# Performance work log

Measured on AMD Instinct MI355X. Metric: run time of the kernel, lower is better.

Reference implementation:

```python
import jax, jax.numpy as jnp
import numpy as np

B, N, R, VR = 4, 10475, 48, 96


def setup_inputs() -> dict:
    key = jax.random.key(0)
    k1, k2, k3, k4 = jax.random.split(key, 4)
    v1s = jax.random.normal(k1, (B, N, 3), dtype=jnp.float32)
    v2s = jax.random.normal(k2, (B, N, 3), dtype=jnp.float32)
    cmaps = jax.random.randint(k3, (B, R, R), 0, 2).astype(bool)
    rid_to_vid = jax.random.randint(k4, (R, VR), 0, N, dtype=jnp.int32)
    return {"v1s": v1s, "v2s": v2s, "cmaps": cmaps, "rid_to_vid": rid_to_vid}


def reference(v1s, v2s, cmaps, rid_to_vid):
    # Gather region vertex subsets for ALL regions at once: [B, R, Vr, 3]
    g1 = v1s[:, rid_to_vid, :]
    g2 = v2s[:, rid_to_vid, :]
    # Squared norms per point
    sq1 = jnp.sum(g1 * g1, axis=-1)                 # [B, R, Vr]
    sq2 = jnp.sum(g2 * g2, axis=-1)                 # [B, R, Vr]
    # Inner products for every (region r of person1, region s of person2) pair
    inner = jnp.einsum('brvc,bswc->brsvw', g1, g2)  # [B, R, R, Vr, Vr]
    d2 = sq1[:, :, None, :, None] + sq2[:, None, :, None, :] - 2.0 * inner
    d = jnp.sqrt(jnp.maximum(d2, 0.0))              # squared=False -> euclidean
    # min over the two vertex-subset axes -> per region-pair min distance [B, R, R]
    min_d = jnp.min(d, axis=(3, 4))
    # Original averages min dists only over active contact pairs (torch.where(cmap))
    m = cmaps.astype(min_d.dtype)                   # [B, R, R]
    return jnp.sum(min_d * m, axis=(1, 2)) / jnp.sum(m, axis=(1, 2))
```

## Files before the change

### kernel.cpp

```cpp
#include <hip/hip_runtime.h>

#define B_ 4
#define R_ 48
#define VR_ 96
#define NROWS (B_ * 2 * R_)
#define ROWF 288

__global__ __launch_bounds__(256) void gather_kernel(
    const float* __restrict__ v1s, const float* __restrict__ v2s,
    const int* __restrict__ rid_to_vid, float* __restrict__ gbuf, int N) {
  const int i = blockIdx.x * 256 + threadIdx.x;
  if (i >= NROWS * VR_) return;
  const int v = i % VR_;
  const int row = i / VR_;
  const int r = row % R_;
  const int bs = row / R_;
  const int set = bs & 1;
  const int b = bs >> 1;
  const int idx = rid_to_vid[r * VR_ + v];
  const float* src = (set ? v2s : v1s) + ((size_t)b * N + idx) * 3;
  float* dst = gbuf + (size_t)row * ROWF;
  dst[v] = src[0];
  dst[VR_ + v] = src[1];
  dst[2 * VR_ + v] = src[2];
}

__global__ __launch_bounds__(256) void cell_kernel(
    const float* __restrict__ gbuf, float* __restrict__ minbuf) {
  const int bid = blockIdx.x;
  const int b = bid / (R_ * 12);
  const int rem = bid % (R_ * 12);
  const int r = rem / 12;
  const int quad = rem % 12;

  __shared__ float s1[ROWF];
  __shared__ float s2[4 * ROWF];

  const float* g1 = gbuf + (size_t)((b * 2 + 0) * R_ + r) * ROWF;
  const float* g2 = gbuf + (size_t)((b * 2 + 1) * R_ + quad * 4) * ROWF;

  const int t = threadIdx.x;
  const float4* g1v = (const float4*)g1;
  const float4* g2v = (const float4*)g2;
  float4* s1v = (float4*)s1;
  float4* s2v = (float4*)s2;
  if (t < 72) s1v[t] = g1v[t];
  s2v[t] = g2v[t];
  if (t < 32) s2v[256 + t] = g2v[256 + t];
  __syncthreads();

  const int w = t >> 6;
  const int lane = t & 63;
  const float* r2 = s2 + w * ROWF;
  const int hi = lane >> 3;
  const int lo = lane & 7;

  float ax[12], ay[12], az[12];
#pragma unroll
  for (int i = 0; i < 12; ++i) {
    const int vi = hi * 12 + i;
    ax[i] = s1[vi]; ay[i] = s1[VR_ + vi]; az[i] = s1[2 * VR_ + vi];
  }

  float acc[4] = {3.4e38f, 3.4e38f, 3.4e38f, 3.4e38f};
#pragma unroll
  for (int j = 0; j < 12; ++j) {
    const int wj = lo * 12 + j;
    const float bx = r2[wj], by = r2[VR_ + wj], bz = r2[2 * VR_ + wj];
#pragma unroll
    for (int i = 0; i < 12; ++i) {
      const float dx = ax[i] - bx;
      const float dy = ay[i] - by;
      const float dz = az[i] - bz;
      const float d2 = dx * dx + dy * dy + dz * dz;
      acc[i & 3] = fminf(acc[i & 3], d2);
    }
  }
  float mind2 = fminf(fminf(acc[0], acc[1]), fminf(acc[2], acc[3]));
#pragma unroll
  for (int off = 32; off > 0; off >>= 1)
    mind2 = fminf(mind2, __shfl_down(mind2, off, 64));
  if (lane == 0)
    minbuf[(b * R_ + r) * R_ + quad * 4 + w] = sqrtf(fmaxf(mind2, 0.0f));
}

__global__ __launch_bounds__(256) void finalize_kernel(
    const float* __restrict__ min_d, const unsigned char* __restrict__ cm,
    float* __restrict__ out) {
  const int b = blockIdx.x;
  const int t = threadIdx.x;
  const unsigned int* cm32 = (const unsigned int*)cm;

  __shared__ int stride4_s;
  if (t < 64) {
    const unsigned int d = cm32[t];
    const unsigned int b1 = (d >> 8) & 0xff, b2 = (d >> 16) & 0xff, b3 = d >> 24;
    const bool nz = (b1 | b2 | b3) != 0;
    const bool big = (b1 > 1) || (b2 > 1) || (b3 > 1);
    const unsigned long long nzm = __ballot(nz);
    const unsigned long long bigm = __ballot(big);
    if (t == 0) stride4_s = (bigm != 0ull || nzm == 0ull) ? 1 : 0;
  }
  __syncthreads();
  const int stride4 = stride4_s;

  float sum = 0.0f, cnt = 0.0f;
  for (int i = t; i < R_ * R_; i += 256) {
    const int gi = b * R_ * R_ + i;
    const bool m = stride4 ? (cm32[gi] != 0u) : (cm[gi] != 0);
    if (m) { sum += min_d[gi]; cnt += 1.0f; }
  }
#pragma unroll
  for (int off = 32; off > 0; off >>= 1) {
    sum += __shfl_down(sum, off, 64);
    cnt += __shfl_down(cnt, off, 64);
  }
  __shared__ float ws_[4], wc_[4];
  if ((t & 63) == 0) { ws_[t >> 6] = sum; wc_[t >> 6] = cnt; }
  __syncthreads();
  if (t == 0) {
    const float S = ws_[0] + ws_[1] + ws_[2] + ws_[3];
    const float C = wc_[0] + wc_[1] + wc_[2] + wc_[3];
    out[b] = S / C;
  }
}

extern "C" void kernel_launch(void* const* d_in, const int* in_sizes, int n_in,
                              void* d_out, int out_size, void* d_ws, size_t ws_size,
                              hipStream_t stream) {
  const float* v1s = (const float*)d_in[0];
  const float* v2s = (const float*)d_in[1];
  const unsigned char* cmaps = (const unsigned char*)d_in[2];
  const int* rid_to_vid = (const int*)d_in[3];
  float* out = (float*)d_out;

  float* minbuf = (float*)d_ws;
  float* gbuf = (float*)((char*)d_ws + (64 << 10));

  const int N = in_sizes[0] / (B_ * 3);

  gather_kernel<<<(NROWS * VR_ + 255) / 256, 256, 0, stream>>>(v1s, v2s, rid_to_vid, gbuf, N);
  cell_kernel<<<B_ * R_ * 12, 256, 0, stream>>>(gbuf, minbuf);
  finalize_kernel<<<B_, 256, 0, stream>>>(minbuf, cmaps, out);
}
```

Baseline: 26.99 us.

## Skip inactive cells, fuse finalize into cell kernel via last-block reduction

The cell kernel now reads the contact map and computes distance minima only for active region pairs, so work on masked-out cells is skipped. The separate finalize launch is replaced by an atomic counter where the last block performs the masked average. Shared-memory staging is dropped in favour of direct float4 loads into registers, and the inner loop uses packed float2 arithmetic. The mask-format detection moves into the gather kernel, which also resets the counter. In exchange it adds atomics, thread fences and a serial final reduction in one block, and the mask check makes waves within a block diverge.

```diff
diff --git a/kernel.cpp b/kernel.cpp
--- a/kernel.cpp
+++ b/kernel.cpp
@@ -3,13 +3,30 @@
 #define B_ 4
 #define R_ 48
 #define VR_ 96
+#define ROWF 288
 #define NROWS (B_ * 2 * R_)
-#define ROWF 288
+#define NCELL (B_ * R_ * R_)
+#define NBLK_CELL (B_ * R_ * 12)
+
+typedef float v2f __attribute__((ext_vector_type(2)));
+
 
 __global__ __launch_bounds__(256) void gather_kernel(
     const float* __restrict__ v1s, const float* __restrict__ v2s,
-    const int* __restrict__ rid_to_vid, float* __restrict__ gbuf, int N) {
-  const int i = blockIdx.x * 256 + threadIdx.x;
+    const int* __restrict__ rid_to_vid, const unsigned char* __restrict__ cm,
+    float* __restrict__ gbuf, int* __restrict__ ctrl, int N) {
+  const int t = threadIdx.x;
+  if (blockIdx.x == 0 && t < 64) {
+    const unsigned int d = ((const unsigned int*)cm)[t];
+    const unsigned int b1 = (d >> 8) & 0xff, b2 = (d >> 16) & 0xff, b3 = d >> 24;
+    const unsigned long long nzm = __ballot((b1 | b2 | b3) != 0);
+    const unsigned long long bigm = __ballot((b1 > 1) || (b2 > 1) || (b3 > 1));
+    if (t == 0) {
+      ctrl[0] = 0;
+      ctrl[1] = (bigm != 0ull || nzm == 0ull) ? 1 : 0;
+    }
+  }
+  const int i = blockIdx.x * 256 + t;
   if (i >= NROWS * VR_) return;
   const int v = i % VR_;
   const int row = i / VR_;
@@ -26,102 +43,91 @@
 }
 
 __global__ __launch_bounds__(256) void cell_kernel(
-    const float* __restrict__ gbuf, float* __restrict__ minbuf) {
+    const float* __restrict__ gbuf, const unsigned char* __restrict__ cm,
+    float* __restrict__ minbuf, int* __restrict__ ctrl,
+    float* __restrict__ out) {
   const int bid = blockIdx.x;
   const int b = bid / (R_ * 12);
   const int rem = bid % (R_ * 12);
   const int r = rem / 12;
   const int quad = rem % 12;
+  const int t = threadIdx.x;
+  const int w = t >> 6, lane = t & 63;
+  const int s = quad * 4 + w;
+  const int cellIdx = (b * R_ + r) * R_ + s;
 
-  __shared__ float s1[ROWF];
-  __shared__ float s2[4 * ROWF];
+  const int stride4 = ctrl[1];
+  const unsigned int* cm32 = (const unsigned int*)cm;
+  const bool active = stride4 ? (cm32[cellIdx] != 0u) : (cm[cellIdx] != 0);
 
-  const float* g1 = gbuf + (size_t)((b * 2 + 0) * R_ + r) * ROWF;
-  const float* g2 = gbuf + (size_t)((b * 2 + 1) * R_ + quad * 4) * ROWF;
+  if (active) {
+    const float* row1 = gbuf + (size_t)((b * 2 + 0) * R_ + r) * ROWF;
+    const float* row2 = gbuf + (size_t)((b * 2 + 1) * R_ + s) * ROWF;
+    const int hi = lane >> 3, lo = lane & 7;
 
-  const int t = threadIdx.x;
-  const float4* g1v = (const float4*)g1;
-  const float4* g2v = (const float4*)g2;
-  float4* s1v = (float4*)s1;
-  float4* s2v = (float4*)s2;
-  if (t < 72) s1v[t] = g1v[t];
-  s2v[t] = g2v[t];
-  if (t < 32) s2v[256 + t] = g2v[256 + t];
-  __syncthreads();
+    float Ax[12], Ay[12], Az[12];
+    v2f Bx[6], By[6], Bz[6];
+#pragma unroll
+    for (int k = 0; k < 3; ++k) {
+      *(float4*)&Ax[4 * k] = ((const float4*)(row1       + hi * 12))[k];
+      *(float4*)&Ay[4 * k] = ((const float4*)(row1 +  96 + hi * 12))[k];
+      *(float4*)&Az[4 * k] = ((const float4*)(row1 + 192 + hi * 12))[k];
+      *(float4*)&Bx[2 * k] = ((const float4*)(row2       + lo * 12))[k];
+      *(float4*)&By[2 * k] = ((const float4*)(row2 +  96 + lo * 12))[k];
+      *(float4*)&Bz[2 * k] = ((const float4*)(row2 + 192 + lo * 12))[k];
+    }
 
-  const int w = t >> 6;
-  const int lane = t & 63;
-  const float* r2 = s2 + w * ROWF;
-  const int hi = lane >> 3;
-  const int lo = lane & 7;
-
-  float ax[12], ay[12], az[12];
+    float acc[4] = {3.4e38f, 3.4e38f, 3.4e38f, 3.4e38f};
 #pragma unroll
-  for (int i = 0; i < 12; ++i) {
-    const int vi = hi * 12 + i;
-    ax[i] = s1[vi]; ay[i] = s1[VR_ + vi]; az[i] = s1[2 * VR_ + vi];
+    for (int i = 0; i < 12; ++i) {
+      const v2f axx = {Ax[i], Ax[i]};
+      const v2f ayy = {Ay[i], Ay[i]};
+      const v2f azz = {Az[i], Az[i]};
+#pragma unroll
+      for (int j = 0; j < 6; ++j) {
+        const v2f dx = axx - Bx[j];
+        const v2f dy = ayy - By[j];
+        const v2f dz = azz - Bz[j];
+        const v2f d2 = dx * dx + dy * dy + dz * dz;
+        acc[j & 3] = fminf(acc[j & 3], fminf(d2.x, d2.y));
+      }
+    }
+    float mind2 = fminf(fminf(acc[0], acc[1]), fminf(acc[2], acc[3]));
+#pragma unroll
+    for (int off = 32; off > 0; off >>= 1)
+      mind2 = fminf(mind2, __shfl_down(mind2, off, 64));
+    if (lane == 0) {
+      atomicExch(&minbuf[cellIdx], sqrtf(fmaxf(mind2, 0.0f)));
+      __threadfence();
+    }
   }
 
-  float acc[4] = {3.4e38f, 3.4e38f, 3.4e38f, 3.4e38f};
+  __syncthreads();
+  __shared__ int lastflag;
+  if (t == 0) lastflag = (atomicAdd(&ctrl[0], 1) == NBLK_CELL - 1) ? 1 : 0;
+  __syncthreads();
+  if (!lastflag) return;
+
+  __threadfence();
+  __shared__ float ws_[4], wc_[4];
+  for (int bb = 0; bb < B_; ++bb) {
+    float sum = 0.0f, cnt = 0.0f;
+    for (int i = t; i < R_ * R_; i += 256) {
+      const int gi = bb * R_ * R_ + i;
+      const bool m = stride4 ? (cm32[gi] != 0u) : (cm[gi] != 0);
+      if (m) { sum += minbuf[gi]; cnt += 1.0f; }
+    }
 #pragma unroll
-  for (int j = 0; j < 12; ++j) {
-    const int wj = lo * 12 + j;
-    const float bx = r2[wj], by = r2[VR_ + wj], bz = r2[2 * VR_ + wj];
-#pragma unroll
-    for (int i = 0; i < 12; ++i) {
-      const float dx = ax[i] - bx;
-      const float dy = ay[i] - by;
-      const float dz = az[i] - bz;
-      const float d2 = dx * dx + dy * dy + dz * dz;
-      acc[i & 3] = fminf(acc[i & 3], d2);
+    for (int off = 32; off > 0; off >>= 1) {
+      sum += __shfl_down(sum, off, 64);
+      cnt += __shfl_down(cnt, off, 64);
     }
-  }
-  float mind2 = fminf(fminf(acc[0], acc[1]), fminf(acc[2], acc[3]));
-#pragma unroll
-  for (int off = 32; off > 0; off >>= 1)
-    mind2 = fminf(mind2, __shfl_down(mind2, off, 64));
-  if (lane == 0)
-    minbuf[(b * R_ + r) * R_ + quad * 4 + w] = sqrtf(fmaxf(mind2, 0.0f));
-}
-
-__global__ __launch_bounds__(256) void finalize_kernel(
-    const float* __restrict__ min_d, const unsigned char* __restrict__ cm,
-    float* __restrict__ out) {
-  const int b = blockIdx.x;
-  const int t = threadIdx.x;
-  const unsigned int* cm32 = (const unsigned int*)cm;
-
-  __shared__ int stride4_s;
-  if (t < 64) {
-    const unsigned int d = cm32[t];
-    const unsigned int b1 = (d >> 8) & 0xff, b2 = (d >> 16) & 0xff, b3 = d >> 24;
-    const bool nz = (b1 | b2 | b3) != 0;
-    const bool big = (b1 > 1) || (b2 > 1) || (b3 > 1);
-    const unsigned long long nzm = __ballot(nz);
-    const unsigned long long bigm = __ballot(big);
-    if (t == 0) stride4_s = (bigm != 0ull || nzm == 0ull) ? 1 : 0;
-  }
-  __syncthreads();
-  const int stride4 = stride4_s;
-
-  float sum = 0.0f, cnt = 0.0f;
-  for (int i = t; i < R_ * R_; i += 256) {
-    const int gi = b * R_ * R_ + i;
-    const bool m = stride4 ? (cm32[gi] != 0u) : (cm[gi] != 0);
-    if (m) { sum += min_d[gi]; cnt += 1.0f; }
-  }
-#pragma unroll
-  for (int off = 32; off > 0; off >>= 1) {
-    sum += __shfl_down(sum, off, 64);
-    cnt += __shfl_down(cnt, off, 64);
-  }
-  __shared__ float ws_[4], wc_[4];
-  if ((t & 63) == 0) { ws_[t >> 6] = sum; wc_[t >> 6] = cnt; }
-  __syncthreads();
-  if (t == 0) {
-    const float S = ws_[0] + ws_[1] + ws_[2] + ws_[3];
-    const float C = wc_[0] + wc_[1] + wc_[2] + wc_[3];
-    out[b] = S / C;
+    if ((t & 63) == 0) { ws_[t >> 6] = sum; wc_[t >> 6] = cnt; }
+    __syncthreads();
+    if (t == 0)
+      out[bb] = (ws_[0] + ws_[1] + ws_[2] + ws_[3]) /
+                (wc_[0] + wc_[1] + wc_[2] + wc_[3]);
+    __syncthreads();
   }
 }
 
@@ -135,11 +141,12 @@
   float* out = (float*)d_out;
 
   float* minbuf = (float*)d_ws;
+  int* ctrl = (int*)((char*)d_ws + 40960);
   float* gbuf = (float*)((char*)d_ws + (64 << 10));
 
   const int N = in_sizes[0] / (B_ * 3);
 
-  gather_kernel<<<(NROWS * VR_ + 255) / 256, 256, 0, stream>>>(v1s, v2s, rid_to_vid, gbuf, N);
-  cell_kernel<<<B_ * R_ * 12, 256, 0, stream>>>(gbuf, minbuf);
-  finalize_kernel<<<B_, 256, 0, stream>>>(minbuf, cmaps, out);
+  gather_kernel<<<(NROWS * VR_ + 255) / 256, 256, 0, stream>>>(
+      v1s, v2s, rid_to_vid, cmaps, gbuf, ctrl, N);
+  cell_kernel<<<NBLK_CELL, 256, 0, stream>>>(gbuf, cmaps, minbuf, ctrl, out);
 }
```

Measured after the change: 102.4 us. 3.79x slower.
